# Optimization experiments

Measured on AMD Instinct MI355X. Metric: run time of the kernel, lower is better.

The kernel has to match this reference:

```python
import jax, jax.numpy as jnp
import numpy as np

L, B, DM, H, HID, NSPK, NB, NC, WIN = 128, 64, 1024, 256, 256, 2, 30, 6, 10
F = 2 * H            # biLSTM output feature dim
MEM = F + HID        # concat of node features and graph-conv output
R = 2 * NSPK * NSPK  # number of edge relations


def _build_edges():
    src_l, dst_l = [], []
    for j in range(L):
        for k in range(max(0, j - WIN), min(L, j + WIN + 1)):
            dst_l.append(j); src_l.append(k)
    dst = np.asarray(dst_l, np.int32); src = np.asarray(src_l, np.int32)
    offs = (np.arange(B, dtype=np.int32) * L)[:, None]
    edge_dst = (dst[None] + offs).reshape(-1)
    edge_src = (src[None] + offs).reshape(-1)
    mask = np.zeros((L, L), bool); mask[dst, src] = True
    return edge_src, edge_dst, mask


def setup_inputs():
    key = jax.random.key(0)
    ks = iter(jax.random.split(key, 32))
    rn = lambda *s: jax.random.normal(next(ks), s, jnp.float32) * 0.05
    edge_src, edge_dst, edge_mask = _build_edges()
    return {
        'U': jax.random.normal(next(ks), (L, B, DM), jnp.float32),
        'umask': jnp.ones((B, L), jnp.float32),
        'Wih0': rn(2, 4 * H, DM), 'Whh0': rn(2, 4 * H, H), 'b0': rn(2, 4 * H),
        'Wih1': rn(2, 4 * H, F), 'Whh1': rn(2, 4 * H, H), 'b1': rn(2, 4 * H),
        'W_scalar': rn(F, L),
        'basis': rn(NB, F, HID), 'comp': rn(R, NB),
        'W_root': rn(F, HID), 'b_rgcn': rn(HID),
        'gc_W1': rn(HID, HID), 'gc_W2': rn(HID, HID), 'gc_b': rn(HID),
        'Wm': rn(MEM, MEM), 'bm': rn(MEM),
        'Wl': rn(MEM, HID), 'bl': rn(HID),
        'Ws': rn(HID, NC), 'bs': rn(NC),
        'speakers': jax.random.randint(next(ks), (L, B), 0, NSPK, jnp.int32),
        'edge_src': jnp.asarray(edge_src), 'edge_dst': jnp.asarray(edge_dst),
        'edge_mask': jnp.asarray(edge_mask),
    }


def _lstm_dir(x, Wih, Whh, b, reverse):
    Bx, Hh = x.shape[1], Whh.shape[1]
    def step(carry, xt):
        h, c = carry
        g = xt @ Wih.T + h @ Whh.T + b          # PyTorch gate order i,f,g,o
        i, f, gg, o = jnp.split(g, 4, axis=-1)
        c = jax.nn.sigmoid(f) * c + jax.nn.sigmoid(i) * jnp.tanh(gg)
        h = jax.nn.sigmoid(o) * jnp.tanh(c)
        return (h, c), h
    init = (jnp.zeros((Bx, Hh), x.dtype), jnp.zeros((Bx, Hh), x.dtype))
    return jax.lax.scan(step, init, x, reverse=reverse)[1]


def _bilstm(x, Wih, Whh, b):
    return jnp.concatenate([_lstm_dir(x, Wih[0], Whh[0], b[0], False),
                            _lstm_dir(x, Wih[1], Whh[1], b[1], True)], -1)


def reference(U, umask, Wih0, Whh0, b0, Wih1, Whh1, b1, W_scalar, basis, comp,
              W_root, b_rgcn, gc_W1, gc_W2, gc_b, Wm, bm, Wl, bl, Ws, bs,
              speakers, edge_src, edge_dst, edge_mask):
    # --- 2-layer biLSTM encoder ---
    feats = _bilstm(_bilstm(U, Wih0, Whh0, b0), Wih1, Whh1, b1)   # (L,B,F)
    # --- MaskedEdgeAttention ('attn1'): edge weights ---
    scale = jnp.einsum('sbd,dm->sbm', feats, W_scalar)            # (L,B,L)
    alpha = jax.nn.softmax(scale, axis=0).transpose(1, 2, 0)      # (B,Lt,Ls)
    masked = alpha * jnp.where(edge_mask, 1.0, 1e-10)
    scores = masked / masked.sum(-1, keepdims=True) * edge_mask
    b_idx = edge_dst // L; i0 = edge_dst % L; i1 = edge_src % L
    edge_norm = scores[b_idx, i0, i1]                             # (E,)
    # --- edge types: speaker pair + temporal direction ---
    s_dst = speakers[i0, b_idx]; s_src = speakers[i1, b_idx]
    e_dir = jnp.where(i0 < i1, 0, 1)
    edge_type = s_dst * (2 * NSPK) + s_src * 2 + e_dir            # (E,) in [0,R)
    # --- node features, conversation-major ---
    x = feats.transpose(1, 0, 2).reshape(B * L, F)                # (N,F)
    N = B * L
    # --- RGCNConv with basis decomposition ---
    W_rel = jnp.einsum('rb,bfo->rfo', comp, basis)                # (R,F,HID)
    x_rel = jnp.einsum('nf,rfo->nro', x, W_rel)                   # (N,R,HID)
    msg = x_rel[edge_src, edge_type] * edge_norm[:, None]
    h = jax.ops.segment_sum(msg, edge_dst, num_segments=N) + x @ W_root + b_rgcn
    # --- GraphConv ---
    agg = jax.ops.segment_sum(h[edge_src], edge_dst, num_segments=N)
    h2 = h @ gc_W1 + gc_b + agg @ gc_W2                           # (N,HID)
    em = jnp.concatenate([x, h2], -1)                             # (N,MEM)
    em = em.reshape(B, L, MEM).transpose(1, 0, 2)                 # (L,B,MEM)
    # --- MatchingAttention ('general2') at every timestep, vectorized ---
    um = umask.T                                                  # (L,B)
    x_tr = em @ Wm + bm                                           # (L,B,MEM)
    logits = jnp.einsum('tbm,sbm->tbs', x_tr, em * um[:, :, None]) * umask[None]
    a = jax.nn.softmax(jnp.tanh(logits), axis=2) * umask[None]
    a = a / a.sum(2, keepdims=True)
    att = jnp.einsum('tbs,sbm->tbm', a, em)
    hidden = jax.nn.relu(att @ Wl + bl)                           # dropout = eval identity
    logp = jax.nn.log_softmax(hidden @ Ws + bs, axis=2)           # (L,B,NC)
    return logp.transpose(1, 0, 2).reshape(B * L, NC)
```

## Files before the change

kernel.cpp:

```cpp
#include <hip/hip_runtime.h>
#include <cstdint>


typedef __attribute__((ext_vector_type(8))) short bf16x8;
typedef __attribute__((ext_vector_type(4))) float f32x4;

__device__ __forceinline__ void gload_lds16(const void* g, void* l) {
  __builtin_amdgcn_global_load_lds(
      (const __attribute__((address_space(1))) void*)g,
      (__attribute__((address_space(3))) void*)l, 16, 0, 0);
}

template<bool HASBIAS, bool ACCUM, bool RELU, bool OUTBF>
__global__ __launch_bounds__(256) void gemm_bf16_nt(
    const ushort* __restrict__ A, const ushort* __restrict__ Bt,
    const float* __restrict__ bias, void* __restrict__ Cv,
    int M, int N, int K, long lda, long ldc,
    long sA, long sB, long sC, long sBias)
{
  const int bz = blockIdx.z;
  A += (long)bz * sA;
  Bt += (long)bz * sB;
  if (HASBIAS) bias += (long)bz * sBias;
  float*  Cf = OUTBF ? nullptr : ((float*)Cv + (long)bz * sC);
  ushort* Cb = OUTBF ? ((ushort*)Cv + (long)bz * sC) : nullptr;

  const int bn = blockIdx.x * 128, bm = blockIdx.y * 128;

  __shared__ ushort As[128][32];
  __shared__ ushort Bs[128][32];

  const int tid = threadIdx.x;
  const int wave = tid >> 6, lane = tid & 63;
  const int wm = (wave >> 1) * 64, wn = (wave & 1) * 64;
  const int fr = lane & 15;
  const int fk = (lane >> 4) * 8;

  f32x4 acc[4][4];
#pragma unroll
  for (int i = 0; i < 4; ++i)
#pragma unroll
    for (int j = 0; j < 4; ++j) acc[i][j] = (f32x4){0.f, 0.f, 0.f, 0.f};

  const int f0 = wave * 2 * 64 + lane;
  const int f1 = f0 + 64;
  const int r0 = f0 >> 2, c0 = (f0 & 3) * 8;
  const int r1 = f1 >> 2, c1 = (f1 & 3) * 8;
  ushort* As0 = (ushort*)As + wave * 2 * 512;
  ushort* As1 = As0 + 512;
  ushort* Bs0 = (ushort*)Bs + wave * 2 * 512;
  ushort* Bs1 = Bs0 + 512;

  for (int k0 = 0; k0 < K; k0 += 32) {
    gload_lds16(A + (long)(bm + r0) * lda + k0 + c0, As0);
    gload_lds16(A + (long)(bm + r1) * lda + k0 + c1, As1);
    gload_lds16(Bt + (long)(bn + r0) * K + k0 + c0, Bs0);
    gload_lds16(Bt + (long)(bn + r1) * K + k0 + c1, Bs1);
    __syncthreads();

    bf16x8 af[4], bfr[4];
#pragma unroll
    for (int f = 0; f < 4; ++f) {
      af[f]  = *(const bf16x8*)&As[wm + f * 16 + fr][fk];
      bfr[f] = *(const bf16x8*)&Bs[wn + f * 16 + fr][fk];
    }
#pragma unroll
    for (int mf = 0; mf < 4; ++mf)
#pragma unroll
      for (int nf = 0; nf < 4; ++nf)
        acc[mf][nf] = __builtin_amdgcn_mfma_f32_16x16x32_bf16(
            af[mf], bfr[nf], acc[mf][nf], 0, 0, 0);
    __syncthreads();
  }

  float bv[4];
#pragma unroll
  for (int nf = 0; nf < 4; ++nf)
    bv[nf] = HASBIAS ? bias[bn + wn + nf * 16 + fr] : 0.f;

  const int crow0 = (lane >> 4) * 4;
#pragma unroll
  for (int mf = 0; mf < 4; ++mf)
#pragma unroll
    for (int r = 0; r < 4; ++r) {
      const long roff = (long)(bm + wm + mf * 16 + crow0 + r) * ldc + bn + wn;
#pragma unroll
      for (int nf = 0; nf < 4; ++nf) {
        float v = acc[mf][nf][r] + bv[nf];
        if (OUTBF) {
          unsigned u = __float_as_uint(v);
          u += 0x7fffu + ((u >> 16) & 1u);
          Cb[roff + nf * 16 + fr] = (ushort)(u >> 16);
        } else {
          if (ACCUM) v += Cf[roff + nf * 16 + fr];
          if (RELU) v = fmaxf(v, 0.f);
          Cf[roff + nf * 16 + fr] = v;
        }
      }
    }
}

__device__ __forceinline__ unsigned short f2bf(float f) {
  unsigned u = __float_as_uint(f);
  u += 0x7fffu + ((u >> 16) & 1u);
  return (unsigned short)(u >> 16);
}
__device__ __forceinline__ float bf2f(ushort v) {
  return __uint_as_float(((unsigned)v) << 16);
}
__device__ __forceinline__ float fast_sig(float x) {
  return __builtin_amdgcn_rcpf(1.f + __expf(-x));
}
__device__ __forceinline__ float fast_tanh(float x) {
  return 2.f * fast_sig(2.f * x) - 1.f;
}

__device__ __forceinline__ int sdot4_(uint a, uint b, int c) {
#if __has_builtin(__builtin_amdgcn_sdot4)
  return __builtin_amdgcn_sdot4((int)a, (int)b, c, false);
#else
  int r = c;
  r += ((int)(a << 24) >> 24) * ((int)(b << 24) >> 24);
  r += ((int)(a << 16) >> 24) * ((int)(b << 16) >> 24);
  r += ((int)(a << 8)  >> 24) * ((int)(b << 8)  >> 24);
  r += ((int)a >> 24)         * ((int)b >> 24);
  return r;
#endif
}

__global__ __launch_bounds__(256) void cvt_all_k(
    const float* __restrict__ U, ushort* __restrict__ ubf,
    const float* __restrict__ W0, ushort* __restrict__ w0,
    const float* __restrict__ W1, ushort* __restrict__ w1)
{
  const int bid = blockIdx.x;
  const float* src; ushort* dst; long base;
  if (bid < 8192)       { src = U;  dst = ubf; base = (long)bid * 1024; }
  else if (bid < 10240) { src = W0; dst = w0;  base = (long)(bid - 8192) * 1024; }
  else                  { src = W1; dst = w1;  base = (long)(bid - 10240) * 1024; }
  const long i = base + threadIdx.x * 4;
  float4 v = *(const float4*)(src + i);
  ushort4 o;
  o.x = f2bf(v.x); o.y = f2bf(v.y); o.z = f2bf(v.z); o.w = f2bf(v.w);
  *(ushort4*)(dst + i) = o;
}

__global__ __launch_bounds__(256) void tp_all_k(
    const float* __restrict__ s0, ushort* __restrict__ d0,
    const float* __restrict__ s1, const float* __restrict__ s2,
    ushort* __restrict__ d12,
    const float* __restrict__ s3, ushort* __restrict__ d3,
    const float* __restrict__ s4, ushort* __restrict__ d4,
    const float* __restrict__ s5, ushort* __restrict__ d5)
{
  __shared__ float tile[32][33];
  const int bid = blockIdx.x;
  const float* src; ushort* dst; int C, gx, local, dstStride, dstOff;
  if (bid < 128)       { src = s0; dst = d0;  C = 256; gx = 8;  local = bid;        dstStride = 512; dstOff = 0; }
  else if (bid < 192)  { src = s1; dst = d12; C = 256; gx = 8;  local = bid - 128;  dstStride = 512; dstOff = 0; }
  else if (bid < 256)  { src = s2; dst = d12; C = 256; gx = 8;  local = bid - 192;  dstStride = 512; dstOff = 256; }
  else if (bid < 832)  { src = s3; dst = d3;  C = 768; gx = 24; local = bid - 256;  dstStride = 768; dstOff = 0; }
  else if (bid < 1024) { src = s4; dst = d4;  C = 256; gx = 8;  local = bid - 832;  dstStride = 768; dstOff = 0; }
  else                 { src = s5; dst = d5;  C = 128; gx = 4;  local = bid - 1024; dstStride = 512; dstOff = 0; }
  const int c0 = (local % gx) * 32, r0 = (local / gx) * 32;
  const int tx = threadIdx.x & 31, ty = threadIdx.x >> 5;
#pragma unroll
  for (int j = 0; j < 4; ++j)
    tile[ty + j * 8][tx] = src[(long)(r0 + ty + j * 8) * C + c0 + tx];
  __syncthreads();
#pragma unroll
  for (int j = 0; j < 4; ++j)
    dst[(long)(c0 + ty + j * 8) * dstStride + dstOff + r0 + tx] = f2bf(tile[tx][ty + j * 8]);
}

__global__ __launch_bounds__(256) void pack_whh_all_k(
    const float* __restrict__ Whh0, const float* __restrict__ Whh1,
    uint* __restrict__ Wq, float* __restrict__ fscale)
{
  const int wid = (blockIdx.x * 256 + threadIdx.x) >> 6;
  const int lane = threadIdx.x & 63;
  const int l = wid >> 11;
  const int wid2 = wid & 2047;
  const int d = wid2 >> 10, gi = wid2 & 1023;
  const float* Whh = l ? Whh1 : Whh0;
  const float* row = Whh + ((long)d * 1024 + gi) * 256 + lane * 4;
  float v0 = row[0], v1 = row[1], v2 = row[2], v3 = row[3];
  float am = fmaxf(fmaxf(fabsf(v0), fabsf(v1)), fmaxf(fabsf(v2), fabsf(v3)));
#pragma unroll
  for (int off = 32; off > 0; off >>= 1) am = fmaxf(am, __shfl_xor(am, off, 64));
  am = fmaxf(am, 1e-12f);
  const float inv = 127.f / am;
  int q0 = __float2int_rn(v0 * inv), q1 = __float2int_rn(v1 * inv);
  int q2 = __float2int_rn(v2 * inv), q3 = __float2int_rn(v3 * inv);
  uint w = (uint)(q0 & 255) | ((uint)(q1 & 255) << 8) |
           ((uint)(q2 & 255) << 16) | ((uint)(q3 & 255) << 24);
  Wq[(long)l * 131072 + ((long)d * 64 + lane) * 1024 + gi] = w;
  if (lane == 0) fscale[l * 2048 + d * 1024 + gi] = am / 127.f;
}

__global__ __launch_bounds__(1024) void lstm4_k(
    const float* __restrict__ Xg,
    const uint* __restrict__ Wq,
    const float* __restrict__ fscale,
    ushort* __restrict__ out,
    int bmajor, long ldo)
{
  const int bx = blockIdx.x;
  const int d = bx >> 6, b = bx & 63;
  const int tid = threadIdx.x;

  __shared__ uint hq[2][64];
  __shared__ float preactF[1024];

  uint w[64];
  const uint* wrow = Wq + (long)d * 65536 + tid;
#pragma unroll
  for (int k4 = 0; k4 < 64; ++k4) w[k4] = wrow[k4 * 1024];

  if (tid < 128) ((uint*)hq)[tid] = 0u;

  const float fsc = fscale[d * 1024 + tid] * (1.0f / 127.0f);
  const float* Xd = Xg + (long)d * 8192 * 1024;

  float c = 0.f;
  float x0 = 0.f, x1 = 0.f, x2 = 0.f, x3 = 0.f;
  if (tid < 256) {
    const float* xr = Xd + ((long)((d ? 127 : 0) * 64 + b)) * 1024;
    x0 = xr[tid]; x1 = xr[tid + 256]; x2 = xr[tid + 512]; x3 = xr[tid + 768];
  }
  __syncthreads();

  int cur = 0;
  for (int step = 0; step < 128; ++step) {
    const int t = d ? 127 - step : step;

    float n0 = 0.f, n1 = 0.f, n2 = 0.f, n3 = 0.f;
    if (tid < 256 && step + 1 < 128) {
      const float* xr = Xd + ((long)((d ? 126 - step : step + 1) * 64 + b)) * 1024;
      n0 = xr[tid]; n1 = xr[tid + 256]; n2 = xr[tid + 512]; n3 = xr[tid + 768];
    }

    int acc = 0;
    const uint4* hrow = (const uint4*)hq[cur];
#pragma unroll
    for (int k16 = 0; k16 < 16; ++k16) {
      uint4 h4 = hrow[k16];
      acc = sdot4_(w[k16 * 4 + 0], h4.x, acc);
      acc = sdot4_(w[k16 * 4 + 1], h4.y, acc);
      acc = sdot4_(w[k16 * 4 + 2], h4.z, acc);
      acc = sdot4_(w[k16 * 4 + 3], h4.w, acc);
    }
    preactF[tid] = (float)acc * fsc;
    __syncthreads();

    if (tid < 256) {
      float p0 = x0 + preactF[tid];
      float p1 = x1 + preactF[tid + 256];
      float p2 = x2 + preactF[tid + 512];
      float p3 = x3 + preactF[tid + 768];
      const float ig = fast_sig(p0), fg = fast_sig(p1);
      const float gg = fast_tanh(p2), og = fast_sig(p3);
      c = fg * c + ig * gg;
      const float h = og * fast_tanh(c);
      const long row = bmajor ? ((long)b * 128 + t) : ((long)t * 64 + b);
      out[row * ldo + (d << 8) + tid] = f2bf(h);
      ((char*)hq[cur ^ 1])[tid] = (char)__float2int_rn(h * 127.f);
      x0 = n0; x1 = n1; x2 = n2; x3 = n3;
    }
    __syncthreads();
    cur ^= 1;
  }
}

__global__ __launch_bounds__(256) void wrel_k(const float* __restrict__ basis,
                                              const float* __restrict__ comp,
                                              ushort* __restrict__ wrel2t) {
  const int f = blockIdx.x;
  const int o = threadIdx.x;
  __shared__ float cs[240];
  if (o < 240) cs[o] = comp[o];
  __syncthreads();
  float acc[8];
#pragma unroll
  for (int r = 0; r < 8; ++r) acc[r] = 0.f;
  for (int bb = 0; bb < 30; ++bb) {
    const float v = basis[((long)bb * 512 + f) * 256 + o];
#pragma unroll
    for (int r = 0; r < 8; ++r) acc[r] = fmaf(cs[r * 30 + bb], v, acc[r]);
  }
#pragma unroll
  for (int r = 0; r < 8; ++r)
    wrel2t[((long)(r * 256 + o)) * 512 + f] = f2bf(acc[r]);
}

__global__ __launch_bounds__(256) void rgcn_fused_k(
    const float* __restrict__ scale, const ushort* __restrict__ xrel,
    const float* __restrict__ hroot, const int* __restrict__ spk,
    ushort* __restrict__ hagg)
{
  const int n = blockIdx.x;
  const int b = n >> 7, t = n & 127;
  const int o = threadIdx.x;
  const int lo = max(t - 10, 0), hi = min(t + 10, 127);
  const int cnt = hi - lo + 1;

  __shared__ float sc[128], red[128];
  __shared__ int spks[21];
  __shared__ int spkt_s;

  if (o < 128) {
    const float v = scale[((long)(b * 128 + o)) * 128 + t];
    sc[o] = v; red[o] = v;
  }
  if (o == 0) spkt_s = spk[t * 64 + b];
  if (o >= 128 && o - 128 < cnt) spks[o - 128] = spk[(lo + o - 128) * 64 + b];
  __syncthreads();
  for (int off = 64; off > 0; off >>= 1) {
    if (o < off) red[o] = fmaxf(red[o], red[o + off]);
    __syncthreads();
  }
  const float m = red[0];
  __syncthreads();
  if (o < 128) {
    const float e = expf(sc[o] - m);
    sc[o] = e;
    const int dd = o - t;
    const bool inwin = (dd <= 10) && (dd >= -10);
    red[o] = e * (inwin ? 1.0f : 1e-10f);
  }
  __syncthreads();
  for (int off = 64; off > 0; off >>= 1) {
    if (o < off) red[o] += red[o + off];
    __syncthreads();
  }
  const float inv_msum = 1.0f / red[0];
  __syncthreads();

  const int spkt = spkt_s;
  float acc = hroot[(long)n * 256 + o];
  for (int q = 0; q < cnt; ++q) {
    const int s = lo + q;
    const float wv = sc[s] * inv_msum;
    const int et = spkt * 4 + spks[q] * 2 + ((t < s) ? 0 : 1);
    acc = fmaf(bf2f(xrel[(((long)(b * 128 + s)) * 8 + et) * 256 + o]), wv, acc);
  }
  hagg[(long)n * 512 + o] = f2bf(acc);
}

__global__ __launch_bounds__(256) void agg_k(ushort* __restrict__ hagg) {
  const int n = blockIdx.x;
  const int b = n >> 7, t = n & 127;
  const int o = threadIdx.x;
  const int lo = max(t - 10, 0), hi = min(t + 10, 127);
  float acc = 0.f;
  for (int s = lo; s <= hi; ++s) acc += bf2f(hagg[((long)(b * 128 + s)) * 512 + o]);
  hagg[(long)n * 512 + 256 + o] = f2bf(acc);
}

__global__ __launch_bounds__(256) void emt_k(const ushort* __restrict__ src,
                                             ushort* __restrict__ dst) {
  __shared__ ushort tile[32][33];
  const int c0 = blockIdx.x * 32;
  const int r0 = blockIdx.y * 32;
  const int b = blockIdx.z;
  const ushort* s = src + (long)b * 98304;
  ushort* d = dst + (long)b * 98304;
  const int tx = threadIdx.x & 31, ty = threadIdx.x >> 5;
#pragma unroll
  for (int j = 0; j < 4; ++j)
    tile[ty + j * 8][tx] = s[(long)(r0 + ty + j * 8) * 768 + c0 + tx];
  __syncthreads();
#pragma unroll
  for (int j = 0; j < 4; ++j)
    d[(long)(c0 + ty + j * 8) * 128 + r0 + tx] = tile[tx][ty + j * 8];
}

__global__ __launch_bounds__(128) void match_softmax_k(const float* __restrict__ logits,
                                                       const float* __restrict__ umask,
                                                       ushort* __restrict__ abf) {
  const int bx = blockIdx.x;
  const int b = bx >> 7;
  const int s = threadIdx.x;
  __shared__ float red[128];
  const float* row = logits + (long)bx * 128;
  const float um = umask[b * 128 + s];
  const float v = tanhf(row[s] * um * um);
  red[s] = v; __syncthreads();
  for (int off = 64; off > 0; off >>= 1) { if (s < off) red[s] = fmaxf(red[s], red[s + off]); __syncthreads(); }
  const float m = red[0]; __syncthreads();
  const float e = expf(v - m);
  red[s] = e; __syncthreads();
  for (int off = 64; off > 0; off >>= 1) { if (s < off) red[s] += red[s + off]; __syncthreads(); }
  const float es = red[0]; __syncthreads();
  const float p = (e / es) * um;
  red[s] = p; __syncthreads();
  for (int off = 64; off > 0; off >>= 1) { if (s < off) red[s] += red[s + off]; __syncthreads(); }
  const float ps = red[0];
  abf[(long)bx * 128 + s] = f2bf(p / ps);
}

__global__ __launch_bounds__(256) void final_k(const float* __restrict__ hidden,
                                               const float* __restrict__ Ws,
                                               const float* __restrict__ bs,
                                               float* __restrict__ out) {
  __shared__ float wsl[256 * 6];
  const int tid = threadIdx.x;
#pragma unroll
  for (int j = 0; j < 6; ++j) wsl[tid * 6 + j] = Ws[tid * 6 + j];
  __syncthreads();
  const int wave = tid >> 6, lane = tid & 63;
  const int n = blockIdx.x * 4 + wave;
  const float4 hv = *(const float4*)&hidden[(long)n * 256 + lane * 4];
  const float hvv[4] = {hv.x, hv.y, hv.z, hv.w};
  float a[6];
#pragma unroll
  for (int c = 0; c < 6; ++c) a[c] = 0.f;
#pragma unroll
  for (int j = 0; j < 4; ++j)
#pragma unroll
    for (int c = 0; c < 6; ++c)
      a[c] = fmaf(hvv[j], wsl[(lane * 4 + j) * 6 + c], a[c]);
#pragma unroll
  for (int off = 32; off > 0; off >>= 1)
#pragma unroll
    for (int c = 0; c < 6; ++c)
      a[c] += __shfl_xor(a[c], off, 64);
  if (lane == 0) {
    float v[6], m = -1e30f;
#pragma unroll
    for (int c = 0; c < 6; ++c) { v[c] = a[c] + bs[c]; m = fmaxf(m, v[c]); }
    float sum = 0.f;
#pragma unroll
    for (int c = 0; c < 6; ++c) sum += expf(v[c] - m);
    const float lse = m + logf(sum);
#pragma unroll
    for (int c = 0; c < 6; ++c) out[(long)n * 6 + c] = v[c] - lse;
  }
}

extern "C" void kernel_launch(void* const* d_in, const int* in_sizes, int n_in,
                              void* d_out, int out_size, void* d_ws, size_t ws_size,
                              hipStream_t stream) {
  const float* U        = (const float*)d_in[0];
  const float* umask    = (const float*)d_in[1];
  const float* Wih0     = (const float*)d_in[2];
  const float* Whh0     = (const float*)d_in[3];
  const float* b0       = (const float*)d_in[4];
  const float* Wih1     = (const float*)d_in[5];
  const float* Whh1     = (const float*)d_in[6];
  const float* b1       = (const float*)d_in[7];
  const float* W_scalar = (const float*)d_in[8];
  const float* basis    = (const float*)d_in[9];
  const float* comp     = (const float*)d_in[10];
  const float* W_root   = (const float*)d_in[11];
  const float* b_rgcn   = (const float*)d_in[12];
  const float* gc_W1    = (const float*)d_in[13];
  const float* gc_W2    = (const float*)d_in[14];
  const float* gc_b     = (const float*)d_in[15];
  const float* Wm       = (const float*)d_in[16];
  const float* bm       = (const float*)d_in[17];
  const float* Wl       = (const float*)d_in[18];
  const float* bl       = (const float*)d_in[19];
  const float* Wsw      = (const float*)d_in[20];
  const float* bsw      = (const float*)d_in[21];
  const int*   speakers = (const int*)d_in[22];

  float* ws = (float*)d_ws;
  float* gates   = ws + 0L;
  float* feats   = ws + 16777216L;
  float* xbuf    = ws + 20971520L;
  float* feats0  = ws + 25165824L;
  float* scaleb  = ws + 29360128L;
  float* scoresb = ws + 30408704L;
  float* wrelr   = ws + 31457280L;
  float* hroot   = ws + 32505856L;
  uint*  wq      = (uint*)(ws + 34603008L);
  float* fsc     = ws + 34865152L;
  float* wTr     = ws + 34869248L;

  ushort* ubf    = (ushort*)xbuf;
  ushort* wih0bf = (ushort*)feats;
  ushort* wih1bf = (ushort*)(feats + 1048576L);
  ushort* f0bf   = (ushort*)feats0;
  ushort* xemb   = (ushort*)feats0;
  ushort* wrel2t = (ushort*)wrelr;
  ushort* wroott = (ushort*)wTr;
  ushort* gcW12t = wroott + 131072L;
  ushort* Wmt    = gcW12t + 131072L;
  ushort* Wlt    = Wmt + 589824L;
  ushort* wscT   = (ushort*)scoresb;

  ushort* hagg    = (ushort*)xbuf;
  ushort* emT     = (ushort*)xbuf;
  ushort* xrelbf  = (ushort*)gates;
  ushort* xtrbf   = (ushort*)gates;
  ushort* abf     = (ushort*)scoresb;
  ushort* attbf   = (ushort*)feats;

  float*  logitsb = scaleb;
  float*  hiddenb = scaleb;

  pack_whh_all_k<<<1024, 256, 0, stream>>>(Whh0, Whh1, wq, fsc);
  cvt_all_k<<<11264, 256, 0, stream>>>(U, ubf, Wih0, wih0bf, Wih1, wih1bf);
  tp_all_k<<<1088, 256, 0, stream>>>(W_root, wroott, gc_W1, gc_W2, gcW12t,
                                     Wm, Wmt, Wl, Wlt, W_scalar, wscT);
  wrel_k<<<512, 256, 0, stream>>>(basis, comp, wrel2t);

  gemm_bf16_nt<true, false, false, false><<<dim3(8, 64, 2), 256, 0, stream>>>(
      ubf, wih0bf, b0, gates, 8192, 1024, 1024, 1024L, 1024L,
      0L, 1048576L, 8388608L, 1024L);
  lstm4_k<<<128, 1024, 0, stream>>>(gates, wq, fsc, f0bf, 0, 512L);

  gemm_bf16_nt<true, false, false, false><<<dim3(8, 64, 2), 256, 0, stream>>>(
      f0bf, wih1bf, b1, gates, 8192, 1024, 512, 512L, 1024L,
      0L, 524288L, 8388608L, 1024L);
  lstm4_k<<<128, 1024, 0, stream>>>(gates, wq + 131072, fsc + 2048, xemb, 1, 768L);

  gemm_bf16_nt<false, false, false, false><<<dim3(1, 64, 1), 256, 0, stream>>>(
      xemb, wscT, nullptr, scaleb, 8192, 128, 512, 768L, 128L, 0L, 0L, 0L, 0L);
  gemm_bf16_nt<true, false, false, false><<<dim3(2, 64, 1), 256, 0, stream>>>(
      xemb, wroott, b_rgcn, hroot, 8192, 256, 512, 768L, 256L, 0L, 0L, 0L, 0L);
  gemm_bf16_nt<false, false, false, true><<<dim3(16, 64, 1), 256, 0, stream>>>(
      xemb, wrel2t, nullptr, xrelbf, 8192, 2048, 512, 768L, 2048L, 0L, 0L, 0L, 0L);
  rgcn_fused_k<<<8192, 256, 0, stream>>>(scaleb, xrelbf, hroot, speakers, hagg);

  agg_k<<<8192, 256, 0, stream>>>(hagg);
  gemm_bf16_nt<true, false, false, true><<<dim3(2, 64, 1), 256, 0, stream>>>(
      hagg, gcW12t, gc_b, xemb + 512, 8192, 256, 512, 512L, 768L, 0L, 0L, 0L, 0L);

  gemm_bf16_nt<true, false, false, true><<<dim3(6, 64, 1), 256, 0, stream>>>(
      xemb, Wmt, bm, xtrbf, 8192, 768, 768, 768L, 768L, 0L, 0L, 0L, 0L);
  emt_k<<<dim3(24, 4, 64), 256, 0, stream>>>(xemb, emT);
  gemm_bf16_nt<false, false, false, false><<<dim3(1, 1, 64), 256, 0, stream>>>(
      xtrbf, xemb, nullptr, logitsb, 128, 128, 768, 768L, 128L,
      98304L, 98304L, 16384L, 0L);
  match_softmax_k<<<8192, 128, 0, stream>>>(logitsb, umask, abf);
  gemm_bf16_nt<false, false, false, true><<<dim3(6, 1, 64), 256, 0, stream>>>(
      abf, emT, nullptr, attbf, 128, 768, 128, 128L, 768L,
      16384L, 98304L, 98304L, 0L);

  gemm_bf16_nt<true, false, true, false><<<dim3(2, 64, 1), 256, 0, stream>>>(
      attbf, Wlt, bl, hiddenb, 8192, 256, 768, 768L, 256L, 0L, 0L, 0L, 0L);
  final_k<<<2048, 256, 0, stream>>>(hiddenb, Wsw, bsw, (float*)d_out);
}
```

Before: 611.1 us.

## Store LSTM gate pre-activations in bf16 and merge scalar/root GEMMs

The input-projection GEMMs now write the LSTM gate pre-activations as bf16 instead of fp32, and the recurrent kernel reads and widens them. This halves the gate write and read traffic, at some precision cost. The W_scalar and W_root projections are also combined into one GEMM with a concatenated weight and a padded bias vector, so xemb is read once and one launch is removed. The RGCN kernel reads both results from the strided combined buffer.

Result: faster. 584.1 us (-4.4%).

```diff
diff --git a/kernel.cpp b/kernel.cpp
--- a/kernel.cpp
+++ b/kernel.cpp
@@ -131,9 +131,15 @@
 __global__ __launch_bounds__(256) void cvt_all_k(
     const float* __restrict__ U, ushort* __restrict__ ubf,
     const float* __restrict__ W0, ushort* __restrict__ w0,
-    const float* __restrict__ W1, ushort* __restrict__ w1)
+    const float* __restrict__ W1, ushort* __restrict__ w1,
+    const float* __restrict__ b_rgcn, float* __restrict__ biasSW)
 {
   const int bid = blockIdx.x;
+  if (bid >= 11264) {
+    const int idx = (bid - 11264) * 256 + threadIdx.x;
+    if (idx < 384) biasSW[idx] = (idx < 128) ? 0.f : b_rgcn[idx - 128];
+    return;
+  }
   const float* src; ushort* dst; long base;
   if (bid < 8192)       { src = U;  dst = ubf; base = (long)bid * 1024; }
   else if (bid < 10240) { src = W0; dst = w0;  base = (long)(bid - 8192) * 1024; }
@@ -199,7 +205,7 @@
 }
 
 __global__ __launch_bounds__(1024) void lstm4_k(
-    const float* __restrict__ Xg,
+    const ushort* __restrict__ Xg,
     const uint* __restrict__ Wq,
     const float* __restrict__ fscale,
     ushort* __restrict__ out,
@@ -220,13 +226,14 @@
   if (tid < 128) ((uint*)hq)[tid] = 0u;
 
   const float fsc = fscale[d * 1024 + tid] * (1.0f / 127.0f);
-  const float* Xd = Xg + (long)d * 8192 * 1024;
+  const ushort* Xd = Xg + (long)d * 8192 * 1024;
 
   float c = 0.f;
   float x0 = 0.f, x1 = 0.f, x2 = 0.f, x3 = 0.f;
   if (tid < 256) {
-    const float* xr = Xd + ((long)((d ? 127 : 0) * 64 + b)) * 1024;
-    x0 = xr[tid]; x1 = xr[tid + 256]; x2 = xr[tid + 512]; x3 = xr[tid + 768];
+    const ushort* xr = Xd + ((long)((d ? 127 : 0) * 64 + b)) * 1024;
+    x0 = bf2f(xr[tid]); x1 = bf2f(xr[tid + 256]);
+    x2 = bf2f(xr[tid + 512]); x3 = bf2f(xr[tid + 768]);
   }
   __syncthreads();
 
@@ -236,8 +243,9 @@
 
     float n0 = 0.f, n1 = 0.f, n2 = 0.f, n3 = 0.f;
     if (tid < 256 && step + 1 < 128) {
-      const float* xr = Xd + ((long)((d ? 126 - step : step + 1) * 64 + b)) * 1024;
-      n0 = xr[tid]; n1 = xr[tid + 256]; n2 = xr[tid + 512]; n3 = xr[tid + 768];
+      const ushort* xr = Xd + ((long)((d ? 126 - step : step + 1) * 64 + b)) * 1024;
+      n0 = bf2f(xr[tid]); n1 = bf2f(xr[tid + 256]);
+      n2 = bf2f(xr[tid + 512]); n3 = bf2f(xr[tid + 768]);
     }
 
     int acc = 0;
@@ -294,9 +302,8 @@
 }
 
 __global__ __launch_bounds__(256) void rgcn_fused_k(
-    const float* __restrict__ scale, const ushort* __restrict__ xrel,
-    const float* __restrict__ hroot, const int* __restrict__ spk,
-    ushort* __restrict__ hagg)
+    const float* __restrict__ scaleM, const ushort* __restrict__ xrel,
+    const int* __restrict__ spk, ushort* __restrict__ hagg)
 {
   const int n = blockIdx.x;
   const int b = n >> 7, t = n & 127;
@@ -309,7 +316,7 @@
   __shared__ int spkt_s;
 
   if (o < 128) {
-    const float v = scale[((long)(b * 128 + o)) * 128 + t];
+    const float v = scaleM[((long)(b * 128 + o)) * 384 + t];
     sc[o] = v; red[o] = v;
   }
   if (o == 0) spkt_s = spk[t * 64 + b];
@@ -337,7 +344,7 @@
   __syncthreads();
 
   const int spkt = spkt_s;
-  float acc = hroot[(long)n * 256 + o];
+  float acc = scaleM[(long)n * 384 + 128 + o];
   for (int q = 0; q < cnt; ++q) {
     const int s = lo + q;
     const float wv = sc[s] * inv_msum;
@@ -473,10 +480,10 @@
   float* scaleb  = ws + 29360128L;
   float* scoresb = ws + 30408704L;
   float* wrelr   = ws + 31457280L;
-  float* hroot   = ws + 32505856L;
   uint*  wq      = (uint*)(ws + 34603008L);
   float* fsc     = ws + 34865152L;
   float* wTr     = ws + 34869248L;
+  float* biasSW  = ws + 35426304L;
 
   ushort* ubf    = (ushort*)xbuf;
   ushort* wih0bf = (ushort*)feats;
@@ -484,12 +491,13 @@
   ushort* f0bf   = (ushort*)feats0;
   ushort* xemb   = (ushort*)feats0;
   ushort* wrel2t = (ushort*)wrelr;
-  ushort* wroott = (ushort*)wTr;
-  ushort* gcW12t = wroott + 131072L;
+  ushort* wswr   = (ushort*)wTr;
+  ushort* gcW12t = wswr + 196608L;
   ushort* Wmt    = gcW12t + 131072L;
   ushort* Wlt    = Wmt + 589824L;
-  ushort* wscT   = (ushort*)scoresb;
-
+
+  ushort* gatesbf = (ushort*)gates;
+  float*  scaleM  = gates + 8388608L;
   ushort* hagg    = (ushort*)xbuf;
   ushort* emT     = (ushort*)xbuf;
   ushort* xrelbf  = (ushort*)gates;
@@ -501,28 +509,27 @@
   float*  hiddenb = scaleb;
 
   pack_whh_all_k<<<1024, 256, 0, stream>>>(Whh0, Whh1, wq, fsc);
-  cvt_all_k<<<11264, 256, 0, stream>>>(U, ubf, Wih0, wih0bf, Wih1, wih1bf);
-  tp_all_k<<<1088, 256, 0, stream>>>(W_root, wroott, gc_W1, gc_W2, gcW12t,
-                                     Wm, Wmt, Wl, Wlt, W_scalar, wscT);
+  cvt_all_k<<<11266, 256, 0, stream>>>(U, ubf, Wih0, wih0bf, Wih1, wih1bf,
+                                       b_rgcn, biasSW);
+  tp_all_k<<<1088, 256, 0, stream>>>(W_root, wswr + 65536L, gc_W1, gc_W2, gcW12t,
+                                     Wm, Wmt, Wl, Wlt, W_scalar, wswr);
   wrel_k<<<512, 256, 0, stream>>>(basis, comp, wrel2t);
 
-  gemm_bf16_nt<true, false, false, false><<<dim3(8, 64, 2), 256, 0, stream>>>(
-      ubf, wih0bf, b0, gates, 8192, 1024, 1024, 1024L, 1024L,
+  gemm_bf16_nt<true, false, false, true><<<dim3(8, 64, 2), 256, 0, stream>>>(
+      ubf, wih0bf, b0, gatesbf, 8192, 1024, 1024, 1024L, 1024L,
       0L, 1048576L, 8388608L, 1024L);
-  lstm4_k<<<128, 1024, 0, stream>>>(gates, wq, fsc, f0bf, 0, 512L);
-
-  gemm_bf16_nt<true, false, false, false><<<dim3(8, 64, 2), 256, 0, stream>>>(
-      f0bf, wih1bf, b1, gates, 8192, 1024, 512, 512L, 1024L,
+  lstm4_k<<<128, 1024, 0, stream>>>(gatesbf, wq, fsc, f0bf, 0, 512L);
+
+  gemm_bf16_nt<true, false, false, true><<<dim3(8, 64, 2), 256, 0, stream>>>(
+      f0bf, wih1bf, b1, gatesbf, 8192, 1024, 512, 512L, 1024L,
       0L, 524288L, 8388608L, 1024L);
-  lstm4_k<<<128, 1024, 0, stream>>>(gates, wq + 131072, fsc + 2048, xemb, 1, 768L);
-
-  gemm_bf16_nt<false, false, false, false><<<dim3(1, 64, 1), 256, 0, stream>>>(
-      xemb, wscT, nullptr, scaleb, 8192, 128, 512, 768L, 128L, 0L, 0L, 0L, 0L);
-  gemm_bf16_nt<true, false, false, false><<<dim3(2, 64, 1), 256, 0, stream>>>(
-      xemb, wroott, b_rgcn, hroot, 8192, 256, 512, 768L, 256L, 0L, 0L, 0L, 0L);
+  lstm4_k<<<128, 1024, 0, stream>>>(gatesbf, wq + 131072, fsc + 2048, xemb, 1, 768L);
+
+  gemm_bf16_nt<true, false, false, false><<<dim3(3, 64, 1), 256, 0, stream>>>(
+      xemb, wswr, biasSW, scaleM, 8192, 384, 512, 768L, 384L, 0L, 0L, 0L, 0L);
   gemm_bf16_nt<false, false, false, true><<<dim3(16, 64, 1), 256, 0, stream>>>(
       xemb, wrel2t, nullptr, xrelbf, 8192, 2048, 512, 768L, 2048L, 0L, 0L, 0L, 0L);
-  rgcn_fused_k<<<8192, 256, 0, stream>>>(scaleb, xrelbf, hroot, speakers, hagg);
+  rgcn_fused_k<<<8192, 256, 0, stream>>>(scaleM, xrelbf, speakers, hagg);
 
   agg_k<<<8192, 256, 0, stream>>>(hagg);
   gemm_bf16_nt<true, false, false, true><<<dim3(2, 64, 1), 256, 0, stream>>>(
```
